# Performance work log

Measured on AMD Instinct MI355X. Metric: run time of the kernel, lower is better.

## Reference

```python
import jax, jax.numpy as jnp
import numpy as np

N = 100000   # num nodes
E = 1600000  # num edges
D = 64       # feature / hidden dim (irreps_in == hidden_dim)
SCALE = D ** -0.5


def setup_inputs() -> dict:
    key = jax.random.key(0)
    ks = jax.random.split(key, 6)
    x = jax.random.normal(ks[0], (N, D), dtype=jnp.float32)
    edge_index = jax.random.randint(ks[1], (2, E), 0, N, dtype=jnp.int32)
    std = D ** -0.5
    Wq = jax.random.normal(ks[2], (D, D), dtype=jnp.float32) * std
    Wk = jax.random.normal(ks[3], (D, D), dtype=jnp.float32) * std
    Wv = jax.random.normal(ks[4], (D, D), dtype=jnp.float32) * std
    Wo = jax.random.normal(ks[5], (D, D), dtype=jnp.float32) * std
    return {"x": x, "edge_index": edge_index, "Wq": Wq, "Wk": Wk, "Wv": Wv, "Wo": Wo}


def reference(x, edge_index, Wq, Wk, Wv, Wo):
    # Per-receiver variable-length attention over incoming neighbors.
    # Mathematically identical to the torch module's degree-bucketed SDPA
    # (softmax over each node's neighbor set), without padding buffers.
    sender, receiver = edge_index[0], edge_index[1]
    Q = x @ Wq  # [N, D]
    K = x @ Wk
    V = x @ Wv
    # per-edge logits: <Q[receiver], K[sender]> * scale
    s = jnp.einsum('ed,ed->e', Q[receiver], K[sender]) * SCALE  # [E]
    # numerically stable segment softmax over receiver groups
    m = jax.ops.segment_max(s, receiver, num_segments=N)  # -inf for empty segments
    m_safe = jnp.where(jnp.isfinite(m), m, 0.0)
    p = jnp.exp(s - m_safe[receiver])  # [E]
    denom = jax.ops.segment_sum(p, receiver, num_segments=N)  # [N]
    num = jax.ops.segment_sum(p[:, None] * V[sender], receiver, num_segments=N)  # [N, D]
    # zero-degree nodes get out = 0 (matches torch: skipped buckets + nan_to_num)
    out = jnp.where(denom[:, None] > 0,
                    num / jnp.maximum(denom, 1e-30)[:, None],
                    0.0)
    return x + out @ Wo
```

## Files before the change

### kernel.cpp

```cpp
#include <hip/hip_runtime.h>
#include <hip/hip_bf16.h>

#define DIM 64
#define SCALE 0.125f
#define BINSH 5
#define NPB 32
#define BCAP 768
#define DBSH 8
#define NDB 256
#define CBCAP 4864
#define CHUNKA 8192
#define MAXCB 400

static __device__ __forceinline__ unsigned int pack2bf(float a, float b) {
    unsigned int ua = __float_as_uint(a), ub = __float_as_uint(b);
    ua += 0x7fffu + ((ua >> 16) & 1u);
    ub += 0x7fffu + ((ub >> 16) & 1u);
    return (ua >> 16) | (ub & 0xffff0000u);
}
static __device__ __forceinline__ float2 unpack2bf(unsigned int u) {
    return make_float2(__uint_as_float(u << 16), __uint_as_float(u & 0xffff0000u));
}

__global__ __launch_bounds__(256) void k_pg(const int* __restrict__ send,
                                            const int* __restrict__ recv,
                                            const float* __restrict__ x,
                                            const float* __restrict__ Wq,
                                            const float* __restrict__ Wk,
                                            const float* __restrict__ Wv,
                                            const float* __restrict__ Wo,
                                            int* __restrict__ bucketCur,
                                            unsigned int* __restrict__ cbuf,
                                            float* __restrict__ Q,
                                            unsigned int* __restrict__ KVb,
                                            int E, int N, int NCB,
                                            int NBA, int nchunk) {
    __shared__ __align__(16) float smem[10240];
    int tid = threadIdx.x;
    int wvv = tid >> 6;
    int lane = tid & 63;

    if ((int)blockIdx.x < NBA) {
        unsigned int* elist = (unsigned int*)smem;
        int* hist  = (int*)(elist + CHUNKA);
        int* lofs  = hist + MAXCB;
        int* gbase = lofs + MAXCB + 1;
        int* lcur  = gbase + MAXCB;
        int* wsum  = lcur + MAXCB;

        int base = blockIdx.x * CHUNKA;
        int lim = min(base + CHUNKA, E);
        int cnt = lim - base;

        for (int i = tid; i < NCB; i += 256) hist[i] = 0;
        __syncthreads();
        for (int i = base + tid; i < lim; i += 256)
            atomicAdd(&hist[recv[i] >> DBSH], 1);
        __syncthreads();

        int i0 = 2 * tid, i1 = 2 * tid + 1;
        int h0 = (i0 < NCB) ? hist[i0] : 0;
        int h1 = (i1 < NCB) ? hist[i1] : 0;
        int ps = h0 + h1;
        int incl = ps;
        for (int o = 1; o < 64; o <<= 1) {
            int t2 = __shfl_up(incl, o, 64);
            if (lane >= o) incl += t2;
        }
        if (lane == 63) wsum[wvv] = incl;
        __syncthreads();
        if (tid == 0) {
            int a = 0;
#pragma unroll
            for (int i2 = 0; i2 < 4; i2++) { int v = wsum[i2]; wsum[i2] = a; a += v; }
        }
        __syncthreads();
        int excl = incl - ps + wsum[wvv];
        if (i0 < NCB) {
            lofs[i0] = excl; lcur[i0] = excl;
            gbase[i0] = h0 ? atomicAdd(&bucketCur[i0], h0) : 0;
        }
        if (i1 < NCB) {
            lofs[i1] = excl + h0; lcur[i1] = excl + h0;
            gbase[i1] = h1 ? atomicAdd(&bucketCur[i1], h1) : 0;
        }
        if (tid == 0) lofs[NCB] = cnt;
        __syncthreads();

        for (int i = base + tid; i < lim; i += 256) {
            int r = recv[i];
            int b = r >> DBSH;
            int p = atomicAdd(&lcur[b], 1);
            elist[p] = (unsigned)send[i] | ((unsigned)(r & (NDB - 1)) << 17);
        }
        __syncthreads();

        for (int i = tid; i < cnt; i += 256) {
            int lo = 0, hi = NCB;
            while (hi - lo > 1) {
                int mid = (lo + hi) >> 1;
                if (lofs[mid] <= i) lo = mid; else hi = mid;
            }
            int pos = gbase[lo] + (i - lofs[lo]);
            if (pos < CBCAP)
                cbuf[(size_t)lo * CBCAP + pos] = elist[i];
        }
        return;
    }

    int qb = blockIdx.x - NBA;
    int m = qb / nchunk;
    int cb = qb % nchunk;
    int base = cb * 256 + wvv * 64;
    int lr = lane >> 3;
    int lc = lane & 7;

    float acc[8][8];
#pragma unroll
    for (int i = 0; i < 8; i++)
#pragma unroll
        for (int j = 0; j < 8; j++) acc[i][j] = 0.f;

    if (m == 2) {
        float* av = smem;
        float* bo = smem + 4096;
        for (int i = tid; i < 1024; i += 256) {
            ((float4*)av)[i] = ((const float4*)Wv)[i];
            ((float4*)bo)[i] = ((const float4*)Wo)[i];
        }
        __syncthreads();
        int rr = tid >> 2, c0 = (tid & 3) * 16;
        float wvo[16];
#pragma unroll
        for (int j = 0; j < 16; j++) wvo[j] = 0.f;
        for (int k = 0; k < 64; k++) {
            float a = av[rr * 64 + k];
#pragma unroll
            for (int j = 0; j < 16; j++)
                wvo[j] = fmaf(a, bo[k * 64 + c0 + j], wvo[j]);
        }
        __syncthreads();
#pragma unroll
        for (int j = 0; j < 16; j++) smem[rr * 64 + c0 + j] = wvo[j];
        __syncthreads();

        if (base < N) {
            float* xw = smem + 4096 + wvv * 1024;
            const float* xp = xw + lr * 8;
#pragma unroll
            for (int h = 0; h < 4; h++) {
#pragma unroll
                for (int c4 = 0; c4 < 4; c4++) {
                    float4 v = make_float4(0.f, 0.f, 0.f, 0.f);
                    if (base + lane < N)
                        v = ((const float4*)x)[(size_t)(base + lane) * 16 + h * 4 + c4];
                    xw[(c4 * 4 + 0) * 64 + lane] = v.x;
                    xw[(c4 * 4 + 1) * 64 + lane] = v.y;
                    xw[(c4 * 4 + 2) * 64 + lane] = v.z;
                    xw[(c4 * 4 + 3) * 64 + lane] = v.w;
                }
                asm volatile("s_waitcnt lgkmcnt(0)" ::: "memory");
                const float* wp = smem + (h * 16) * 64 + lc * 8;
#pragma unroll 4
                for (int kk = 0; kk < 16; kk++) {
                    float4 xa = *(const float4*)(xp + kk * 64);
                    float4 xb = *(const float4*)(xp + kk * 64 + 4);
                    float4 wa = *(const float4*)(wp + kk * 64);
                    float4 wb = *(const float4*)(wp + kk * 64 + 4);
                    float xv[8] = {xa.x, xa.y, xa.z, xa.w, xb.x, xb.y, xb.z, xb.w};
                    float wc[8] = {wa.x, wa.y, wa.z, wa.w, wb.x, wb.y, wb.z, wb.w};
#pragma unroll
                    for (int i = 0; i < 8; i++)
#pragma unroll
                        for (int j = 0; j < 8; j++)
                            acc[i][j] = fmaf(xv[i], wc[j], acc[i][j]);
                }
            }
        }
    } else if (base < N) {
        const float* W = (m == 0) ? Wq : Wk;
        float* xw = smem + wvv * 2048;
        const float* xp = xw + lr * 8;
#pragma unroll
        for (int h = 0; h < 2; h++) {
#pragma unroll
            for (int c4 = 0; c4 < 8; c4++) {
                float4 v = make_float4(0.f, 0.f, 0.f, 0.f);
                if (base + lane < N)
                    v = ((const float4*)x)[(size_t)(base + lane) * 16 + h * 8 + c4];
                xw[(c4 * 4 + 0) * 64 + lane] = v.x;
                xw[(c4 * 4 + 1) * 64 + lane] = v.y;
                xw[(c4 * 4 + 2) * 64 + lane] = v.z;
                xw[(c4 * 4 + 3) * 64 + lane] = v.w;
            }
            asm volatile("s_waitcnt lgkmcnt(0)" ::: "memory");

            const float* wp = W + h * 2048 + lc * 8;
            float4 xa = *(const float4*)(xp);
            float4 xb = *(const float4*)(xp + 4);
            float4 wa0 = *(const float4*)(wp);
            float4 wb0 = *(const float4*)(wp + 4);
            float4 wa1 = *(const float4*)(wp + 64);
            float4 wb1 = *(const float4*)(wp + 68);
#pragma unroll 4
            for (int kk = 0; kk < 32; kk++) {
                float4 xan, xbn, wan, wbn;
                if (kk < 31) {
                    xan = *(const float4*)(xp + (kk + 1) * 64);
                    xbn = *(const float4*)(xp + (kk + 1) * 64 + 4);
                }
                if (kk < 30) {
                    wan = *(const float4*)(wp + (kk + 2) * 64);
                    wbn = *(const float4*)(wp + (kk + 2) * 64 + 4);
                }
                float xv[8] = {xa.x, xa.y, xa.z, xa.w, xb.x, xb.y, xb.z, xb.w};
                float wc[8] = {wa0.x, wa0.y, wa0.z, wa0.w, wb0.x, wb0.y, wb0.z, wb0.w};
#pragma unroll
                for (int i = 0; i < 8; i++)
#pragma unroll
                    for (int j = 0; j < 8; j++)
                        acc[i][j] = fmaf(xv[i], wc[j], acc[i][j]);
                xa = xan; xb = xbn;
                wa0 = wa1; wb0 = wb1;
                wa1 = wan; wb1 = wbn;
            }
        }
    }

    if (base < N) {
#pragma unroll
        for (int i = 0; i < 8; i++) {
            int row = base + lr * 8 + i;
            if (row < N) {
                if (m == 0) {
                    float* dst = &Q[(size_t)row * 64 + lc * 8];
                    ((float4*)dst)[0] = make_float4(acc[i][0], acc[i][1], acc[i][2], acc[i][3]);
                    ((float4*)dst)[1] = make_float4(acc[i][4], acc[i][5], acc[i][6], acc[i][7]);
                } else {
                    unsigned int* dst = &KVb[(size_t)row * 64 + (m - 1) * 32 + lc * 4];
                    uint4 pk;
                    pk.x = pack2bf(acc[i][0], acc[i][1]);
                    pk.y = pack2bf(acc[i][2], acc[i][3]);
                    pk.z = pack2bf(acc[i][4], acc[i][5]);
                    pk.w = pack2bf(acc[i][6], acc[i][7]);
                    *((uint4*)dst) = pk;
                }
            }
        }
    }
}

__global__ __launch_bounds__(256) void k_attn(const float* __restrict__ Q,
                                              const unsigned int* __restrict__ KVb,
                                              const float* __restrict__ x,
                                              const int* __restrict__ bucketCur,
                                              const unsigned int* __restrict__ cbuf,
                                              float* __restrict__ out, int N) {
    __shared__ unsigned int llist[BCAP];
    __shared__ int ldeg[NPB], lofs[NPB + 1], lcur[NPB];
    int tid = threadIdx.x;
    int wvv = tid >> 6;
    int lane = tid & 63;
    int g = lane >> 3;
    int sub = lane & 7;

    int j = blockIdx.x;
    int b = j >> 3;
    int s = j & 7;
    size_t bbase = (size_t)b * CBCAP;
    int cnt = min(bucketCur[b], CBCAP);

    if (tid < NPB) ldeg[tid] = 0;
    __syncthreads();

    for (int i = tid; i < cnt; i += 256) {
        unsigned u = cbuf[bbase + i];
        int n = (u >> 17) & (NDB - 1);
        if ((n >> 5) == s) atomicAdd(&ldeg[n & (NPB - 1)], 1);
    }
    __syncthreads();

    if (wvv == 0 && lane < NPB) {
        int d = ldeg[lane];
        int sc = d;
        for (int o = 1; o < NPB; o <<= 1) {
            int t = __shfl_up(sc, o, NPB);
            if (lane >= o) sc += t;
        }
        lofs[lane + 1] = min(sc, BCAP);
        lcur[lane] = min(sc - d, BCAP);
        if (lane == 0) lofs[0] = 0;
    }
    __syncthreads();

    for (int i = tid; i < cnt; i += 256) {
        unsigned u = cbuf[bbase + i];
        int n = (u >> 17) & (NDB - 1);
        if ((n >> 5) == s) {
            int p = atomicAdd(&lcur[n & (NPB - 1)], 1);
            if (p < BCAP) llist[p] = u & 0x1FFFFu;
        }
    }
    __syncthreads();

    for (int n = wvv; n < NPB; n += 4) {
        int r = (j << BINSH) + n;
        if (r >= N) break;
        int start = lofs[n];
        int end = lofs[n + 1];
        float4 qa = *((const float4*)&Q[(size_t)r * 64 + sub * 8]);
        float4 qb = *((const float4*)&Q[(size_t)r * 64 + sub * 8 + 4]);
        float q[8] = {qa.x, qa.y, qa.z, qa.w, qb.x, qb.y, qb.z, qb.w};
        float acc[8] = {0.f, 0.f, 0.f, 0.f, 0.f, 0.f, 0.f, 0.f};
        float dpart = 0.f;

        int eA = start + g;
        bool vA = eA < end;
        unsigned int sA = vA ? llist[eA] : 0u;
        uint4 kA = *((const uint4*)&KVb[(size_t)sA * 64 + sub * 4]);
        uint4 uA = *((const uint4*)&KVb[(size_t)sA * 64 + 32 + sub * 4]);
        int eB = start + 8 + g;
        bool vB = eB < end;
        unsigned int sB = vB ? llist[eB] : 0u;
        uint4 kB = *((const uint4*)&KVb[(size_t)sB * 64 + sub * 4]);
        uint4 uB = *((const uint4*)&KVb[(size_t)sB * 64 + 32 + sub * 4]);

        for (int bb = start; bb < end; bb += 8) {
            int eC = bb + 16 + g;
            bool vC = eC < end;
            unsigned int sC = vC ? llist[eC] : 0u;
            uint4 kC = *((const uint4*)&KVb[(size_t)sC * 64 + sub * 4]);
            uint4 uC = *((const uint4*)&KVb[(size_t)sC * 64 + 32 + sub * 4]);

            float2 k01 = unpack2bf(kA.x), k23 = unpack2bf(kA.y);
            float2 k45 = unpack2bf(kA.z), k67 = unpack2bf(kA.w);
            float dot = q[0] * k01.x + q[1] * k01.y + q[2] * k23.x + q[3] * k23.y
                      + q[4] * k45.x + q[5] * k45.y + q[6] * k67.x + q[7] * k67.y;
            dot += __shfl_xor(dot, 1);
            dot += __shfl_xor(dot, 2);
            dot += __shfl_xor(dot, 4);
            float w = vA ? __expf(dot * SCALE) : 0.f;

            float2 v01 = unpack2bf(uA.x), v23 = unpack2bf(uA.y);
            float2 v45 = unpack2bf(uA.z), v67 = unpack2bf(uA.w);
            acc[0] = fmaf(w, v01.x, acc[0]);
            acc[1] = fmaf(w, v01.y, acc[1]);
            acc[2] = fmaf(w, v23.x, acc[2]);
            acc[3] = fmaf(w, v23.y, acc[3]);
            acc[4] = fmaf(w, v45.x, acc[4]);
            acc[5] = fmaf(w, v45.y, acc[5]);
            acc[6] = fmaf(w, v67.x, acc[6]);
            acc[7] = fmaf(w, v67.y, acc[7]);
            dpart += w;

            kA = kB; uA = uB; vA = vB;
            kB = kC; uB = uC; vB = vC;
        }

        dpart += __shfl_xor(dpart, 8); dpart += __shfl_xor(dpart, 16); dpart += __shfl_xor(dpart, 32);
#pragma unroll
        for (int jj = 0; jj < 8; jj++) {
            acc[jj] += __shfl_xor(acc[jj], 8);
            acc[jj] += __shfl_xor(acc[jj], 16);
            acc[jj] += __shfl_xor(acc[jj], 32);
        }

        float inv = (dpart > 0.f) ? (1.0f / dpart) : 0.f;

        if (g == 0) {
            float4 xa = *((const float4*)&x[(size_t)r * 64 + sub * 8]);
            float4 xb = *((const float4*)&x[(size_t)r * 64 + sub * 8 + 4]);
            float4 oa = make_float4(fmaf(acc[0], inv, xa.x), fmaf(acc[1], inv, xa.y),
                                    fmaf(acc[2], inv, xa.z), fmaf(acc[3], inv, xa.w));
            float4 ob = make_float4(fmaf(acc[4], inv, xb.x), fmaf(acc[5], inv, xb.y),
                                    fmaf(acc[6], inv, xb.z), fmaf(acc[7], inv, xb.w));
            *((float4*)&out[(size_t)r * 64 + sub * 8]) = oa;
            *((float4*)&out[(size_t)r * 64 + sub * 8 + 4]) = ob;
        }
    }
}


extern "C" void kernel_launch(void* const* d_in, const int* in_sizes, int n_in,
                              void* d_out, int out_size, void* d_ws, size_t ws_size,
                              hipStream_t stream) {
    const float* x  = (const float*)d_in[0];
    const int* edge = (const int*)d_in[1];
    const float* Wq = (const float*)d_in[2];
    const float* Wk = (const float*)d_in[3];
    const float* Wv = (const float*)d_in[4];
    const float* Wo = (const float*)d_in[5];
    float* out = (float*)d_out;

    int N = in_sizes[0] / DIM;
    int E = in_sizes[1] / 2;
    int NBK = (N + NPB - 1) >> BINSH;
    int NCB = (N + NDB - 1) >> DBSH;

    char* p = (char*)d_ws;
    auto cv = [&](size_t bytes) {
        char* r = p;
        p += ((bytes + 255) / 256) * 256;
        return r;
    };
    float*        Q         = (float*)cv((size_t)N * 64 * 4);
    unsigned int* KVb       = (unsigned int*)cv((size_t)N * 64 * 4);
    int*          bucketCur = (int*)cv((size_t)NCB * 4);
    unsigned int* cbuf      = (unsigned int*)cv((size_t)NCB * CBCAP * 4);
    (void)ws_size; (void)n_in; (void)out_size;

    const int* send = edge;
    const int* recv = edge + E;

    int NBA = (E + CHUNKA - 1) / CHUNKA;
    int nchunk = (N + 255) / 256;

    hipMemsetAsync(bucketCur, 0, (size_t)NCB * 4, stream);
    k_pg<<<NBA + 3 * nchunk, 256, 0, stream>>>(send, recv, x, Wq, Wk, Wv, Wo,
                                               bucketCur, cbuf, Q, KVb,
                                               E, N, NCB, NBA, nchunk);
    k_attn<<<NBK, 256, 0, stream>>>(Q, KVb, x, bucketCur, cbuf, out, N);
}
```

Baseline: 246.1 us.

## Add per-bucket grouping kernel so attention reads pre-sorted neighbor lists

Adds a new kernel that sorts each 256-node coarse bucket by receiver in place and writes per-node start offsets and counts. The attention kernel then loads its contiguous slice directly, instead of having each of 8 blocks rescan the whole bucket twice with shared atomics. The scatter step in the partition phase is also changed from a per-element binary search to a per-bucket, per-wave copy. This adds one kernel launch and an extra pass over the bucket data, in exchange for removing the repeated scans in the attention kernel.

After: 240.4 us. -2.3%, faster.

```diff
diff --git a/kernel.cpp b/kernel.cpp
--- a/kernel.cpp
+++ b/kernel.cpp
@@ -35,7 +35,7 @@
                                             unsigned int* __restrict__ KVb,
                                             int E, int N, int NCB,
                                             int NBA, int nchunk) {
-    __shared__ __align__(16) float smem[10240];
+    __shared__ __align__(16) float smem[9808];
     int tid = threadIdx.x;
     int wvv = tid >> 6;
     int lane = tid & 63;
@@ -95,15 +95,15 @@
         }
         __syncthreads();
 
-        for (int i = tid; i < cnt; i += 256) {
-            int lo = 0, hi = NCB;
-            while (hi - lo > 1) {
-                int mid = (lo + hi) >> 1;
-                if (lofs[mid] <= i) lo = mid; else hi = mid;
+        for (int b = wvv; b < NCB; b += 4) {
+            int s0 = lofs[b];
+            int cb2 = lofs[b + 1] - s0;
+            int g = gbase[b];
+            for (int i2 = lane; i2 < cb2; i2 += 64) {
+                int pos = g + i2;
+                if (pos < CBCAP)
+                    cbuf[(size_t)b * CBCAP + pos] = elist[s0 + i2];
             }
-            int pos = gbase[lo] + (i - lofs[lo]);
-            if (pos < CBCAP)
-                cbuf[(size_t)lo * CBCAP + pos] = elist[i];
         }
         return;
     }
@@ -147,13 +147,14 @@
         if (base < N) {
             float* xw = smem + 4096 + wvv * 1024;
             const float* xp = xw + lr * 8;
+            bool rowok = (base + lane) < N;
+            const float4* xrow = (const float4*)x + (size_t)(base + lane) * 16;
+            const float4 z4 = make_float4(0.f, 0.f, 0.f, 0.f);
 #pragma unroll
             for (int h = 0; h < 4; h++) {
 #pragma unroll
                 for (int c4 = 0; c4 < 4; c4++) {
-                    float4 v = make_float4(0.f, 0.f, 0.f, 0.f);
-                    if (base + lane < N)
-                        v = ((const float4*)x)[(size_t)(base + lane) * 16 + h * 4 + c4];
+                    float4 v = rowok ? xrow[h * 4 + c4] : z4;
                     xw[(c4 * 4 + 0) * 64 + lane] = v.x;
                     xw[(c4 * 4 + 1) * 64 + lane] = v.y;
                     xw[(c4 * 4 + 2) * 64 + lane] = v.z;
@@ -250,61 +251,90 @@
     }
 }
 
+__global__ __launch_bounds__(256) void k_grp(const int* __restrict__ bucketCur,
+                                             unsigned int* __restrict__ cbuf,
+                                             int* __restrict__ nstart,
+                                             int* __restrict__ ncount,
+                                             int N) {
+    __shared__ unsigned int elist[CBCAP];
+    __shared__ int ldeg[NDB], lcur[NDB], wsum[4];
+    int tid = threadIdx.x;
+    int wvv = tid >> 6;
+    int lane = tid & 63;
+
+    int b = blockIdx.x;
+    int bbase = b * CBCAP;
+    int cnt = min(bucketCur[b], CBCAP);
+
+    for (int i = tid; i < cnt; i += 256) elist[i] = cbuf[bbase + i];
+    ldeg[tid] = 0;
+    __syncthreads();
+    for (int i = tid; i < cnt; i += 256)
+        atomicAdd(&ldeg[(elist[i] >> 17) & (NDB - 1)], 1);
+    __syncthreads();
+
+    int d = ldeg[tid];
+    int incl = d;
+    for (int o = 1; o < 64; o <<= 1) {
+        int t = __shfl_up(incl, o, 64);
+        if (lane >= o) incl += t;
+    }
+    if (lane == 63) wsum[wvv] = incl;
+    __syncthreads();
+    int woff = 0;
+    for (int w2 = 0; w2 < wvv; w2++) woff += wsum[w2];
+    int start = woff + incl - d;
+    lcur[tid] = start;
+    int r = (b << DBSH) + tid;
+    if (r < N) {
+        nstart[r] = bbase + start;
+        ncount[r] = d;
+    }
+    __syncthreads();
+
+    for (int i = tid; i < cnt; i += 256) {
+        unsigned u = elist[i];
+        int n = (u >> 17) & (NDB - 1);
+        int p = atomicAdd(&lcur[n], 1);
+        cbuf[bbase + p] = u & 0x1FFFFu;
+    }
+}
+
 __global__ __launch_bounds__(256) void k_attn(const float* __restrict__ Q,
                                               const unsigned int* __restrict__ KVb,
                                               const float* __restrict__ x,
-                                              const int* __restrict__ bucketCur,
-                                              const unsigned int* __restrict__ cbuf,
+                                              const int* __restrict__ nstart,
+                                              const int* __restrict__ ncount,
+                                              const unsigned int* __restrict__ nlist,
                                               float* __restrict__ out, int N) {
     __shared__ unsigned int llist[BCAP];
-    __shared__ int ldeg[NPB], lofs[NPB + 1], lcur[NPB];
+    __shared__ int lofs[NPB + 1];
+    __shared__ int sbs;
     int tid = threadIdx.x;
-    int wvv = tid >> 6;
+    int wv = tid >> 6;
     int lane = tid & 63;
     int g = lane >> 3;
     int sub = lane & 7;
 
     int j = blockIdx.x;
-    int b = j >> 3;
-    int s = j & 7;
-    size_t bbase = (size_t)b * CBCAP;
-    int cnt = min(bucketCur[b], CBCAP);
-
-    if (tid < NPB) ldeg[tid] = 0;
-    __syncthreads();
-
-    for (int i = tid; i < cnt; i += 256) {
-        unsigned u = cbuf[bbase + i];
-        int n = (u >> 17) & (NDB - 1);
-        if ((n >> 5) == s) atomicAdd(&ldeg[n & (NPB - 1)], 1);
-    }
-    __syncthreads();
-
-    if (wvv == 0 && lane < NPB) {
-        int d = ldeg[lane];
-        int sc = d;
-        for (int o = 1; o < NPB; o <<= 1) {
-            int t = __shfl_up(sc, o, NPB);
-            if (lane >= o) sc += t;
-        }
-        lofs[lane + 1] = min(sc, BCAP);
-        lcur[lane] = min(sc - d, BCAP);
-        if (lane == 0) lofs[0] = 0;
-    }
-    __syncthreads();
-
-    for (int i = tid; i < cnt; i += 256) {
-        unsigned u = cbuf[bbase + i];
-        int n = (u >> 17) & (NDB - 1);
-        if ((n >> 5) == s) {
-            int p = atomicAdd(&lcur[n & (NPB - 1)], 1);
-            if (p < BCAP) llist[p] = u & 0x1FFFFu;
-        }
-    }
-    __syncthreads();
-
-    for (int n = wvv; n < NPB; n += 4) {
-        int r = (j << BINSH) + n;
+    int r0 = j << BINSH;
+
+    if (tid == 0) sbs = nstart[r0];
+    __syncthreads();
+    int sbase = sbs;
+    if (tid < NPB) {
+        int r = r0 + tid;
+        lofs[tid] = min(nstart[r] - sbase, BCAP);
+        if (tid == NPB - 1)
+            lofs[NPB] = min(nstart[r] + ncount[r] - sbase, BCAP);
+    }
+    __syncthreads();
+    int cnt = lofs[NPB];
+    for (int i = tid; i < cnt; i += 256) llist[i] = nlist[sbase + i];
+    __syncthreads();
+
+    for (int n = wv; n < NPB; n += 4) {
+        int r = r0 + n;
         if (r >= N) break;
         int start = lofs[n];
         int end = lofs[n + 1];
@@ -407,6 +437,8 @@
     unsigned int* KVb       = (unsigned int*)cv((size_t)N * 64 * 4);
     int*          bucketCur = (int*)cv((size_t)NCB * 4);
     unsigned int* cbuf      = (unsigned int*)cv((size_t)NCB * CBCAP * 4);
+    int*          nstart    = (int*)cv((size_t)N * 4);
+    int*          ncount    = (int*)cv((size_t)N * 4);
     (void)ws_size; (void)n_in; (void)out_size;
 
     const int* send = edge;
@@ -419,5 +451,6 @@
     k_pg<<<NBA + 3 * nchunk, 256, 0, stream>>>(send, recv, x, Wq, Wk, Wv, Wo,
                                                bucketCur, cbuf, Q, KVb,
                                                E, N, NCB, NBA, nchunk);
-    k_attn<<<NBK, 256, 0, stream>>>(Q, KVb, x, bucketCur, cbuf, out, N);
-}
+    k_grp<<<NCB, 256, 0, stream>>>(bucketCur, cbuf, nstart, ncount, N);
+    k_attn<<<NBK, 256, 0, stream>>>(Q, KVb, x, nstart, ncount, cbuf, out, N);
+}
```

## Process each 256-node coarse bucket in one 1024-thread attention block

Applied to the files above, without the earlier changes.

The attention kernel used to launch eight 256-thread blocks per coarse bucket, and each block rescanned the whole bucket's edge list from global memory just to keep its own 32 nodes. Now a single 1024-thread block stages the bucket's edges in shared memory once, builds the per-node CSR with a 256-entry scan, and has 16 waves cover the 256 receivers. This removes the eightfold redundant reads of cbuf and the atomics filtering, but it cuts the grid to about 391 blocks and uses more shared memory per block, which may lower occupancy and load balance. It also shrinks the projection kernel's shared array slightly and hoists the x-row pointer and bounds check out of the load loop.

Measured after the change: 236.7 us. -3.8%, faster.

```diff
diff --git a/kernel.cpp b/kernel.cpp
--- a/kernel.cpp
+++ b/kernel.cpp
@@ -3,9 +3,6 @@
 
 #define DIM 64
 #define SCALE 0.125f
-#define BINSH 5
-#define NPB 32
-#define BCAP 768
 #define DBSH 8
 #define NDB 256
 #define CBCAP 4864
@@ -35,7 +32,7 @@
                                             unsigned int* __restrict__ KVb,
                                             int E, int N, int NCB,
                                             int NBA, int nchunk) {
-    __shared__ __align__(16) float smem[10240];
+    __shared__ __align__(16) float smem[9808];
     int tid = threadIdx.x;
     int wvv = tid >> 6;
     int lane = tid & 63;
@@ -147,13 +144,14 @@
         if (base < N) {
             float* xw = smem + 4096 + wvv * 1024;
             const float* xp = xw + lr * 8;
+            bool rowok = (base + lane) < N;
+            const float4* xrow = (const float4*)x + (size_t)(base + lane) * 16;
+            const float4 z4 = make_float4(0.f, 0.f, 0.f, 0.f);
 #pragma unroll
             for (int h = 0; h < 4; h++) {
 #pragma unroll
                 for (int c4 = 0; c4 < 4; c4++) {
-                    float4 v = make_float4(0.f, 0.f, 0.f, 0.f);
-                    if (base + lane < N)
-                        v = ((const float4*)x)[(size_t)(base + lane) * 16 + h * 4 + c4];
+                    float4 v = rowok ? xrow[h * 4 + c4] : z4;
                     xw[(c4 * 4 + 0) * 64 + lane] = v.x;
                     xw[(c4 * 4 + 1) * 64 + lane] = v.y;
                     xw[(c4 * 4 + 2) * 64 + lane] = v.z;
@@ -250,61 +248,67 @@
     }
 }
 
-__global__ __launch_bounds__(256) void k_attn(const float* __restrict__ Q,
-                                              const unsigned int* __restrict__ KVb,
-                                              const float* __restrict__ x,
-                                              const int* __restrict__ bucketCur,
-                                              const unsigned int* __restrict__ cbuf,
-                                              float* __restrict__ out, int N) {
-    __shared__ unsigned int llist[BCAP];
-    __shared__ int ldeg[NPB], lofs[NPB + 1], lcur[NPB];
+__global__ __launch_bounds__(1024) void k_ga(const float* __restrict__ Q,
+                                             const unsigned int* __restrict__ KVb,
+                                             const float* __restrict__ x,
+                                             const int* __restrict__ bucketCur,
+                                             const unsigned int* __restrict__ cbuf,
+                                             float* __restrict__ out, int N) {
+    __shared__ unsigned int elist[CBCAP];
+    __shared__ unsigned int llist[CBCAP];
+    __shared__ int ldeg[NDB], lcur[NDB], lofs[NDB + 1], wsum[4];
     int tid = threadIdx.x;
-    int wvv = tid >> 6;
+    int wv = tid >> 6;
     int lane = tid & 63;
     int g = lane >> 3;
     int sub = lane & 7;
 
-    int j = blockIdx.x;
-    int b = j >> 3;
-    int s = j & 7;
+    int b = blockIdx.x;
     size_t bbase = (size_t)b * CBCAP;
     int cnt = min(bucketCur[b], CBCAP);
 
-    if (tid < NPB) ldeg[tid] = 0;
-    __syncthreads();
-
-    for (int i = tid; i < cnt; i += 256) {
-        unsigned u = cbuf[bbase + i];
+    for (int i = tid; i < cnt; i += 1024) elist[i] = cbuf[bbase + i];
+    if (tid < NDB) ldeg[tid] = 0;
+    __syncthreads();
+    for (int i = tid; i < cnt; i += 1024)
+        atomicAdd(&ldeg[(elist[i] >> 17) & (NDB - 1)], 1);
+    __syncthreads();
+
+    int d = 0, incl = 0;
+    if (tid < NDB) {
+        d = ldeg[tid];
+        incl = d;
+        for (int o = 1; o < 64; o <<= 1) {
+            int t = __shfl_up(incl, o, 64);
+            if (lane >= o) incl += t;
+        }
+        if (lane == 63) wsum[wv] = incl;
+    }
+    __syncthreads();
+    if (tid == 0) {
+        int a = 0;
+#pragma unroll
+        for (int i2 = 0; i2 < 4; i2++) { int v = wsum[i2]; wsum[i2] = a; a += v; }
+    }
+    __syncthreads();
+    if (tid < NDB) {
+        int start = incl - d + wsum[wv];
+        lofs[tid] = start;
+        lcur[tid] = start;
+    }
+    if (tid == 0) lofs[NDB] = cnt;
+    __syncthreads();
+
+    for (int i = tid; i < cnt; i += 1024) {
+        unsigned u = elist[i];
         int n = (u >> 17) & (NDB - 1);
-        if ((n >> 5) == s) atomicAdd(&ldeg[n & (NPB - 1)], 1);
-    }
-    __syncthreads();
-
-    if (wvv == 0 && lane < NPB) {
-        int d = ldeg[lane];
-        int sc = d;
-        for (int o = 1; o < NPB; o <<= 1) {
-            int t = __shfl_up(sc, o, NPB);
-            if (lane >= o) sc += t;
-        }
-        lofs[lane + 1] = min(sc, BCAP);
-        lcur[lane] = min(sc - d, BCAP);
-        if (lane == 0) lofs[0] = 0;
-    }
-    __syncthreads();
-
-    for (int i = tid; i < cnt; i += 256) {
-        unsigned u = cbuf[bbase + i];
-        int n = (u >> 17) & (NDB - 1);
-        if ((n >> 5) == s) {
-            int p = atomicAdd(&lcur[n & (NPB - 1)], 1);
-            if (p < BCAP) llist[p] = u & 0x1FFFFu;
-        }
-    }
-    __syncthreads();
-
-    for (int n = wvv; n < NPB; n += 4) {
-        int r = (j << BINSH) + n;
+        int p = atomicAdd(&lcur[n], 1);
+        llist[p] = u & 0x1FFFFu;
+    }
+    __syncthreads();
+
+    for (int n = wv; n < NDB; n += 16) {
+        int r = (b << DBSH) + n;
         if (r >= N) break;
         int start = lofs[n];
         int end = lofs[n + 1];
@@ -394,7 +398,6 @@
 
     int N = in_sizes[0] / DIM;
     int E = in_sizes[1] / 2;
-    int NBK = (N + NPB - 1) >> BINSH;
     int NCB = (N + NDB - 1) >> DBSH;
 
     char* p = (char*)d_ws;
@@ -419,5 +422,5 @@
     k_pg<<<NBA + 3 * nchunk, 256, 0, stream>>>(send, recv, x, Wq, Wk, Wv, Wo,
                                                bucketCur, cbuf, Q, KVb,
                                                E, N, NCB, NBA, nchunk);
-    k_attn<<<NBK, 256, 0, stream>>>(Q, KVb, x, bucketCur, cbuf, out, N);
+    k_ga<<<NCB, 1024, 0, stream>>>(Q, KVb, x, bucketCur, cbuf, out, N);
 }
```
